# Kernel optimization log

Measured on AMD Instinct MI355X. Metric: run time of the kernel, lower is better.

## Reference

```python
import jax, jax.numpy as jnp
import numpy as np

NUM_CLASSES = 80
NUM_ANCHORS = 3  # len(anchor_mask)
STRIDE = 8.0
# anchors[mask=0,1,2] = (12,16),(19,36),(40,28), divided by stride
ANCHOR_W = jnp.array([12.0, 19.0, 40.0], dtype=jnp.float32) / STRIDE
ANCHOR_H = jnp.array([16.0, 36.0, 28.0], dtype=jnp.float32) / STRIDE


def setup_inputs() -> dict:
    key = jax.random.key(0)
    output = jax.random.normal(key, (16, NUM_ANCHORS * (5 + NUM_CLASSES), 76, 76), dtype=jnp.float32)
    return {"output": output}


def reference(output):
    B, C_total, H, W = output.shape
    A, C = NUM_ANCHORS, NUM_CLASSES
    o = output.reshape(B, A, 5 + C, H, W)

    bxy = jax.nn.sigmoid(o[:, :, 0:2])          # [B,A,2,H,W]
    bwh = jnp.exp(o[:, :, 2:4])                 # [B,A,2,H,W]
    det_confs = jax.nn.sigmoid(o[:, :, 4])      # [B,A,H,W]
    cls_confs = jax.nn.softmax(o[:, :, 5:], axis=2)  # softmax over class dim, [B,A,C,H,W]

    grid_x = jnp.arange(W, dtype=jnp.float32)[None, None, None, :]
    grid_y = jnp.arange(H, dtype=jnp.float32)[None, None, :, None]
    aw = ANCHOR_W[None, :, None, None]
    ah = ANCHOR_H[None, :, None, None]

    bx = (bxy[:, :, 0] + grid_x) / W            # [B,A,H,W]
    by = (bxy[:, :, 1] + grid_y) / H
    bw = (bwh[:, :, 0] * aw) / W
    bh = (bwh[:, :, 1] * ah) / H

    boxes = jnp.stack([bx, by, bw, bh], axis=-1).reshape(B, A * H * W, 4)
    cls_flat = cls_confs.transpose(0, 1, 3, 4, 2).reshape(B, A * H * W, C)
    confs = cls_flat * det_confs.reshape(B, A * H * W, 1)
    return boxes, confs
```

## Files before the change

kernel.cpp:

```cpp
#include <hip/hip_runtime.h>

#define HW_   5776
#define W_    76
#define NC_   80
#define NA_   3
#define NB_   16
#define NPOS  (NB_ * NA_ * HW_)
#define ROWQ  24

__device__ __forceinline__ float sigmoidf_(float x) {
    return 1.0f / (1.0f + __expf(-x));
}

__global__ __launch_bounds__(256) void yolo_kernel(const float* __restrict__ in,
                                                   float* __restrict__ out) {
    __shared__ float4 lds[4][16 * ROWQ];

    const int tid   = threadIdx.x;
    const int lane  = tid & 63;
    const int wv    = tid >> 6;
    const int half  = lane >> 5;
    const int pair  = lane & 31;
    const int Pbase = blockIdx.x * 128 + wv * 32;
    const int P     = Pbase + pair;

    const int slab = P / HW_;
    const int p    = P - slab * HW_;
    const int a    = slab % NA_;

    const float aw3[3] = {1.5f, 2.375f, 5.0f};
    const float ah3[3] = {2.0f, 4.5f, 3.5f};
    const float invW = 1.0f / 76.0f;

    const float* src = in + (size_t)slab * (85 * (size_t)HW_) + p;

    const float b0 = src[0 * (size_t)HW_];
    const float b1 = src[1 * (size_t)HW_];
    const float b2 = src[2 * (size_t)HW_];
    const float b3 = src[3 * (size_t)HW_];
    const float b4 = src[4 * (size_t)HW_];

    const float* csrc = src + (size_t)(5 + half * 40) * HW_;
    float v[40];
#pragma unroll
    for (int c = 0; c < 40; ++c) v[c] = csrc[(size_t)c * HW_];

    const int x = p % W_;
    const int y = p / W_;
    const float bx  = (sigmoidf_(b0) + (float)x) * invW;
    const float by  = (sigmoidf_(b1) + (float)y) * invW;
    const float bw  = __expf(b2) * (aw3[a] * invW);
    const float bh  = __expf(b3) * (ah3[a] * invW);
    const float det = sigmoidf_(b4);

    float m = v[0];
#pragma unroll
    for (int c = 1; c < 40; ++c) m = fmaxf(m, v[c]);
    m = fmaxf(m, __shfl_xor(m, 32));
    float s = 0.0f;
#pragma unroll
    for (int c = 0; c < 40; ++c) { v[c] = __expf(v[c] - m); s += v[c]; }
    s += __shfl_xor(s, 32);
    const float scale = det / s;

    if (half == 0) {
        ((float4*)out)[P] = make_float4(bx, by, bw, bh);
    }

    float4* conf4 = (float4*)out + NPOS + (size_t)Pbase * 20;
    const int myt = pair >> 4;
    const int lp  = pair & 15;
#pragma unroll
    for (int t = 0; t < 2; ++t) {
        if (myt == t) {
#pragma unroll
            for (int i = 0; i < 10; ++i) {
                const int k    = half * 10 + i;
                const int slot = lp * ROWQ + (k ^ (lp & 7));
                lds[wv][slot] = make_float4(v[4*i]   * scale, v[4*i+1] * scale,
                                            v[4*i+2] * scale, v[4*i+3] * scale);
            }
        }
#pragma unroll
        for (int i = 0; i < 5; ++i) {
            const int f    = i * 64 + lane;
            const int lpr  = f / 20;
            const int kq   = f - lpr * 20;
            const int slot = lpr * ROWQ + (kq ^ (lpr & 7));
            conf4[t * 320 + f] = lds[wv][slot];
        }
    }
}

extern "C" void kernel_launch(void* const* d_in, const int* in_sizes, int n_in,
                              void* d_out, int out_size, void* d_ws, size_t ws_size,
                              hipStream_t stream) {
    const float* in = (const float*)d_in[0];
    float* out = (float*)d_out;
    const int nblocks = NPOS / 128;
    yolo_kernel<<<nblocks, 256, 0, stream>>>(in, out);
}
```

Measured before the change: 167.9 us.

## Process four positions per lane with float4 loads in single-wave blocks

```diff
diff --git a/kernel.cpp b/kernel.cpp
--- a/kernel.cpp
+++ b/kernel.cpp
@@ -11,83 +11,110 @@
 __device__ __forceinline__ float sigmoidf_(float x) {
     return 1.0f / (1.0f + __expf(-x));
 }
+__device__ __forceinline__ float getc_(float4 f, int j) {
+    return j == 0 ? f.x : j == 1 ? f.y : j == 2 ? f.z : f.w;
+}
 
-__global__ __launch_bounds__(256) void yolo_kernel(const float* __restrict__ in,
-                                                   float* __restrict__ out) {
-    __shared__ float4 lds[4][16 * ROWQ];
+__global__ __launch_bounds__(64, 1) void yolo_kernel(const float* __restrict__ in,
+                                                     float* __restrict__ out) {
+    __shared__ float4 buf[32 * ROWQ];
 
-    const int tid   = threadIdx.x;
-    const int lane  = tid & 63;
-    const int wv    = tid >> 6;
-    const int half  = lane >> 5;
-    const int pair  = lane & 31;
-    const int Pbase = blockIdx.x * 128 + wv * 32;
-    const int P     = Pbase + pair;
+    const int lane = threadIdx.x;
+    const int half = lane >> 5;
+    const int q    = lane & 31;
 
-    const int slab = P / HW_;
-    const int p    = P - slab * HW_;
+    const int waveP0 = blockIdx.x * 128;
+    const int P0     = waveP0 + q * 4;
+
+    const int slab = P0 / HW_;
+    const int p    = P0 - slab * HW_;
     const int a    = slab % NA_;
 
     const float aw3[3] = {1.5f, 2.375f, 5.0f};
     const float ah3[3] = {2.0f, 4.5f, 3.5f};
     const float invW = 1.0f / 76.0f;
 
-    const float* src = in + (size_t)slab * (85 * (size_t)HW_) + p;
+    const float4* src4 = (const float4*)(in + (size_t)slab * (85 * (size_t)HW_) + p);
+    const int chs = HW_ / 4;
 
-    const float b0 = src[0 * (size_t)HW_];
-    const float b1 = src[1 * (size_t)HW_];
-    const float b2 = src[2 * (size_t)HW_];
-    const float b3 = src[3 * (size_t)HW_];
-    const float b4 = src[4 * (size_t)HW_];
+    const float4 b0 = src4[0 * chs];
+    const float4 b1 = src4[1 * chs];
+    const float4 b2 = src4[2 * chs];
+    const float4 b3 = src4[3 * chs];
+    const float4 b4 = src4[4 * chs];
 
-    const float* csrc = src + (size_t)(5 + half * 40) * HW_;
-    float v[40];
+    const float4* csrc = src4 + (5 + half * 40) * chs;
+    float4 v[40];
 #pragma unroll
-    for (int c = 0; c < 40; ++c) v[c] = csrc[(size_t)c * HW_];
+    for (int c = 0; c < 40; ++c) v[c] = csrc[c * chs];
 
-    const int x = p % W_;
-    const int y = p / W_;
-    const float bx  = (sigmoidf_(b0) + (float)x) * invW;
-    const float by  = (sigmoidf_(b1) + (float)y) * invW;
-    const float bw  = __expf(b2) * (aw3[a] * invW);
-    const float bh  = __expf(b3) * (ah3[a] * invW);
-    const float det = sigmoidf_(b4);
+    float4 m = v[0];
+#pragma unroll
+    for (int c = 1; c < 40; ++c) {
+        m.x = fmaxf(m.x, v[c].x); m.y = fmaxf(m.y, v[c].y);
+        m.z = fmaxf(m.z, v[c].z); m.w = fmaxf(m.w, v[c].w);
+    }
+    m.x = fmaxf(m.x, __shfl_xor(m.x, 32));
+    m.y = fmaxf(m.y, __shfl_xor(m.y, 32));
+    m.z = fmaxf(m.z, __shfl_xor(m.z, 32));
+    m.w = fmaxf(m.w, __shfl_xor(m.w, 32));
+    float4 s = make_float4(0.f, 0.f, 0.f, 0.f);
+#pragma unroll
+    for (int c = 0; c < 40; ++c) {
+        v[c].x = __expf(v[c].x - m.x); s.x += v[c].x;
+        v[c].y = __expf(v[c].y - m.y); s.y += v[c].y;
+        v[c].z = __expf(v[c].z - m.z); s.z += v[c].z;
+        v[c].w = __expf(v[c].w - m.w); s.w += v[c].w;
+    }
+    s.x += __shfl_xor(s.x, 32);
+    s.y += __shfl_xor(s.y, 32);
+    s.z += __shfl_xor(s.z, 32);
+    s.w += __shfl_xor(s.w, 32);
 
-    float m = v[0];
+    const float4 scale = make_float4(sigmoidf_(b4.x) / s.x, sigmoidf_(b4.y) / s.y,
+                                     sigmoidf_(b4.z) / s.z, sigmoidf_(b4.w) / s.w);
+
+    const int x0 = p % W_;
+    const int y  = p / W_;
+    float4* out4 = (float4*)out;
 #pragma unroll
-    for (int c = 1; c < 40; ++c) m = fmaxf(m, v[c]);
-    m = fmaxf(m, __shfl_xor(m, 32));
-    float s = 0.0f;
-#pragma unroll
-    for (int c = 0; c < 40; ++c) { v[c] = __expf(v[c] - m); s += v[c]; }
-    s += __shfl_xor(s, 32);
-    const float scale = det / s;
-
-    if (half == 0) {
-        ((float4*)out)[P] = make_float4(bx, by, bw, bh);
+    for (int jj = 0; jj < 2; ++jj) {
+        const int j = half * 2 + jj;
+        const float bx = (sigmoidf_(getc_(b0, j)) + (float)(x0 + j)) * invW;
+        const float by = (sigmoidf_(getc_(b1, j)) + (float)y) * invW;
+        const float bw = __expf(getc_(b2, j)) * (aw3[a] * invW);
+        const float bh = __expf(getc_(b3, j)) * (ah3[a] * invW);
+        out4[P0 + j] = make_float4(bx, by, bw, bh);
     }
 
-    float4* conf4 = (float4*)out + NPOS + (size_t)Pbase * 20;
-    const int myt = pair >> 4;
-    const int lp  = pair & 15;
+    float4* conf4 = (float4*)out + NPOS + (size_t)waveP0 * 20;
+    const int myt = q >> 3;
 #pragma unroll
-    for (int t = 0; t < 2; ++t) {
+    for (int t = 0; t < 4; ++t) {
         if (myt == t) {
+            const int lpb = (q & 7) * 4;
 #pragma unroll
-            for (int i = 0; i < 10; ++i) {
-                const int k    = half * 10 + i;
-                const int slot = lp * ROWQ + (k ^ (lp & 7));
-                lds[wv][slot] = make_float4(v[4*i]   * scale, v[4*i+1] * scale,
-                                            v[4*i+2] * scale, v[4*i+3] * scale);
+            for (int j = 0; j < 4; ++j) {
+                const int lp = lpb + j;
+                const float sc = getc_(scale, j);
+#pragma unroll
+                for (int i = 0; i < 10; ++i) {
+                    const int k    = half * 10 + i;
+                    const int slot = lp * ROWQ + (k ^ (lp & 7));
+                    buf[slot] = make_float4(getc_(v[4*i],   j) * sc,
+                                            getc_(v[4*i+1], j) * sc,
+                                            getc_(v[4*i+2], j) * sc,
+                                            getc_(v[4*i+3], j) * sc);
+                }
             }
         }
 #pragma unroll
-        for (int i = 0; i < 5; ++i) {
+        for (int i = 0; i < 10; ++i) {
             const int f    = i * 64 + lane;
-            const int lpr  = f / 20;
-            const int kq   = f - lpr * 20;
-            const int slot = lpr * ROWQ + (kq ^ (lpr & 7));
-            conf4[t * 320 + f] = lds[wv][slot];
+            const int lp   = f / 20;
+            const int kq   = f - lp * 20;
+            const int slot = lp * ROWQ + (kq ^ (lp & 7));
+            conf4[t * 640 + f] = buf[slot];
         }
     }
 }
@@ -98,5 +125,5 @@
     const float* in = (const float*)d_in[0];
     float* out = (float*)d_out;
     const int nblocks = NPOS / 128;
-    yolo_kernel<<<nblocks, 256, 0, stream>>>(in, out);
+    yolo_kernel<<<nblocks, 64, 0, stream>>>(in, out);
 }
```

Measured after the change: 171.9 us. 1.02x slower.
